# Kernel tuning notes

Measured on AMD Instinct MI355X. Metric: run time of the kernel, lower is better.

Reference implementation:

```python
import jax, jax.numpy as jnp
import numpy as np

L0, L1, L2 = 32, 16, 8
NS, NB = 512, 256
CUT = 7.0
N, E, G = 16384, 131072, 16
FEAT = L0 + 3 * L1 + 5 * L2  # 120


def setup_inputs() -> dict:
    key = jax.random.key(0)
    ks = jax.random.split(key, 16)
    rn = lambda k, s, sc=1.0: jax.random.normal(k, s, jnp.float32) * sc
    inp = {}
    inp['nodes'] = rn(ks[0], (N, FEAT))
    inp['pos'] = rn(ks[1], (N, 3)) * 5.0
    inp['cell'] = rn(ks[2], (G, 3, 3))
    inp['edge_shift'] = rn(ks[3], (E, 3))
    # tensor-product path weights (e3nn FullyConnectedTensorProduct, uvw mode)
    inp['W0'] = rn(ks[4], (L0, L0, NS))
    inp['W1'] = rn(ks[5], (L1, L1, NS))
    inp['W2'] = rn(ks[6], (L2, L2, NS))
    inp['ln_g'] = jnp.ones((NS,), jnp.float32)
    inp['ln_b'] = jnp.zeros((NS,), jnp.float32)
    inp['df_w1'] = rn(ks[7], (NB, 1024), NB ** -0.5)
    inp['df_b1'] = jnp.zeros((1024,), jnp.float32)
    inp['df_w2'] = rn(ks[8], (1024, NS), 1024 ** -0.5)
    inp['df_b2'] = jnp.zeros((NS,), jnp.float32)
    inp['mi_w1'] = rn(ks[9], (NS, 1024), NS ** -0.5)
    inp['mi_b1'] = jnp.zeros((1024,), jnp.float32)
    inp['mi_w2'] = rn(ks[10], (1024, 1024), 1024 ** -0.5)
    inp['mi_b2'] = jnp.zeros((1024,), jnp.float32)
    inp['mo_w'] = rn(ks[11], (1024, 1), 1024 ** -0.5)
    inp['mo_b'] = jnp.zeros((1,), jnp.float32)
    inp['edge_index'] = jax.random.randint(ks[12], (2, E), 0, N)
    inp['batch_vec'] = jnp.sort(jax.random.randint(ks[13], (N,), 0, G))
    return inp


def _split_irreps(x):
    x0 = x[:, :L0]                                   # (E, L0) scalars 0e
    x1 = x[:, L0:L0 + 3 * L1].reshape(-1, L1, 3)      # (E, L1, 3) vectors 1o
    x2 = x[:, L0 + 3 * L1:].reshape(-1, L2, 5)        # (E, L2, 5) 2e
    return x0, x1, x2


def reference(nodes, pos, cell, edge_shift, W0, W1, W2, ln_g, ln_b,
              df_w1, df_b1, df_w2, df_b2, mi_w1, mi_b1, mi_w2, mi_b2,
              mo_w, mo_b, edge_index, batch_vec):
    src, dst = edge_index[0], edge_index[1]
    # periodic-image translation vector per edge
    bcell = cell[batch_vec[src]]                      # (E,3,3)
    tvec = jnp.einsum('ei,eij->ej', edge_shift, bcell)
    radvec = pos[dst] - pos[src] + tvec               # (E,3)
    dist = jnp.linalg.norm(radvec, axis=1, keepdims=True)  # (E,1)
    r = 1.0 / (dist + 1e-6)
    # Bessel radial embedding with cutoff CUT, NB basis functions
    n = jnp.arange(1, NB + 1, dtype=jnp.float32)
    emb = jnp.sqrt(2.0 / CUT) * jnp.sin(n * jnp.pi * r / CUT) / r  # (E,NB)
    distfilter = jax.nn.silu(emb @ df_w1 + df_b1) @ df_w2 + df_b2  # (E,NS)

    # symmetrized fully-connected tensor product -> 0e scalars
    # 0.5*(tp(xs,xd)+tp(xd,xs)) == contraction of euv with symmetrized W
    xs0, xs1, xs2 = _split_irreps(nodes[src])
    xd0, xd1, xd2 = _split_irreps(nodes[dst])
    fan = jnp.sqrt(jnp.float32(L0 * L0 + L1 * L1 + L2 * L2))  # element path norm
    sym = lambda W: 0.5 * (W + W.transpose(1, 0, 2))
    e0 = jnp.einsum('eu,ev->euv', xs0, xd0)
    mixed = jnp.einsum('euv,uvw->ew', e0, sym(W0)) / fan
    e1 = jnp.einsum('eui,evi->euv', xs1, xd1)
    mixed = mixed + jnp.einsum('euv,uvw->ew', e1, sym(W1)) / (fan * jnp.sqrt(3.0))
    e2 = jnp.einsum('eui,evi->euv', xs2, xd2)
    mixed = mixed + jnp.einsum('euv,uvw->ew', e2, sym(W2)) / (fan * jnp.sqrt(5.0))

    # LayerNorm over numscalars
    mu = jnp.mean(mixed, axis=-1, keepdims=True)
    var = jnp.mean((mixed - mu) ** 2, axis=-1, keepdims=True)
    mixednorm = (mixed - mu) * jax.lax.rsqrt(var + 1e-5) * ln_g + ln_b

    reg = mixednorm * distfilter
    h = jax.nn.silu(reg @ mi_w1 + mi_b1)
    h = jax.nn.silu(h @ mi_w2 + mi_b2)
    return h @ mo_w + mo_b  # (E,1)
```

## Files before the change

kernel.cpp:

```cpp
#include <hip/hip_runtime.h>

#define EE 131072
#define NNODE 16384
#define FEAT 120
#define NS 512
#define NB 256
#define KCAT 1344

typedef unsigned short u16;
typedef __bf16 bf16x8 __attribute__((ext_vector_type(8)));
typedef float f32x4 __attribute__((ext_vector_type(4)));
typedef unsigned short ushort8 __attribute__((ext_vector_type(8)));

__device__ __forceinline__ float b2f(u16 u) {
  union { unsigned int i; float f; } x; x.i = ((unsigned int)u) << 16; return x.f;
}
__device__ __forceinline__ u16 f2b(float f) {
  union { float f; unsigned int i; } x; x.f = f;
  unsigned int lsb = (x.i >> 16) & 1u;
  x.i += 0x7fffu + lsb;
  return (u16)(x.i >> 16);
}
__device__ __forceinline__ u16 f2b_fast(float f) {
  __bf16 h = (__bf16)f;
  union { __bf16 h; u16 u; } x; x.h = h; return x.u;
}
__device__ __forceinline__ float rdany(const void* p, long i, int f32) {
  return f32 ? ((const float*)p)[i] : b2f(((const u16*)p)[i]);
}

__device__ __forceinline__ void gload16(const u16* g, u16* l) {
  __builtin_amdgcn_global_load_lds(
      (__attribute__((address_space(1))) void*)(u16*)g,
      (__attribute__((address_space(3))) void*)l, 16, 0, 0);
}

__global__ void detect_k(const u16* __restrict__ nodes, int* __restrict__ flag) {
  __shared__ int cnt;
  if (threadIdx.x == 0) cnt = 0;
  __syncthreads();
  u16 v = nodes[threadIdx.x];
  int e = (v >> 7) & 0xFF;
  if (e >= 0x48) atomicAdd(&cnt, 1);
  __syncthreads();
  if (threadIdx.x == 0) *flag = (cnt >= 16) ? 1 : 0;
}

__global__ __launch_bounds__(256) void convert_k(const void* __restrict__ src,
                                                 u16* __restrict__ dst, long n,
                                                 const int* __restrict__ flag) {
  long i = (long)blockIdx.x * 256 + threadIdx.x;
  if (i >= n) return;
  if (*flag)
    dst[i] = f2b(((const float*)src)[i]);
  else
    dst[i] = ((const u16*)src)[i];
}

__global__ __launch_bounds__(256) void transpose_k(const u16* __restrict__ in,
                                                   u16* __restrict__ out, int R, int C) {
  __shared__ u16 tile[32][33];
  int c0 = blockIdx.x * 32, r0 = blockIdx.y * 32;
  int tx = threadIdx.x & 31, ty = threadIdx.x >> 5;
  for (int i = 0; i < 32; i += 8) {
    int r = r0 + ty + i, c = c0 + tx;
    if (r < R && c < C) tile[ty + i][tx] = in[(long)r * C + c];
  }
  __syncthreads();
  for (int i = 0; i < 32; i += 8) {
    int r = r0 + tx, c = c0 + ty + i;
    if (r < R && c < C) out[(long)c * R + r] = tile[tx][ty + i];
  }
}

__global__ __launch_bounds__(256) void build_wcat(const u16* __restrict__ W0,
                                                  const u16* __restrict__ W1,
                                                  const u16* __restrict__ W2,
                                                  u16* __restrict__ wcT) {
  int idx = blockIdx.x * 256 + threadIdx.x;
  if (idx >= NS * KCAT) return;
  int w = idx / KCAT, k = idx - w * KCAT;
  const float fan = 36.66060556f;
  float val;
  if (k < 1024) {
    int u = k >> 5, v = k & 31;
    val = 0.5f * (b2f(W0[(u * 32 + v) * NS + w]) + b2f(W0[(v * 32 + u) * NS + w])) / fan;
  } else if (k < 1280) {
    int j = k - 1024;
    int u = j >> 4, v = j & 15;
    val = 0.5f * (b2f(W1[(u * 16 + v) * NS + w]) + b2f(W1[(v * 16 + u) * NS + w])) /
          (fan * 1.7320508076f);
  } else {
    int j = k - 1280;
    int u = j >> 3, v = j & 7;
    val = 0.5f * (b2f(W2[(u * 8 + v) * NS + w]) + b2f(W2[(v * 8 + u) * NS + w])) /
          (fan * 2.2360679775f);
  }
  wcT[idx] = f2b(val);
}

__global__ __launch_bounds__(256) void edge_prep(
    const u16* __restrict__ nodes, const void* __restrict__ pos, const void* __restrict__ cell,
    const void* __restrict__ shift, const int* __restrict__ eidx, const int* __restrict__ batch,
    u16* __restrict__ emb, u16* __restrict__ ocat, int e0, const int* __restrict__ flag) {
  const int wave = threadIdx.x >> 6, lane = threadIdx.x & 63;
  const int el = blockIdx.x * 4 + wave;
  const int e = e0 + el;
  const int f32 = *flag;
  __shared__ u16 sxs[4][FEAT], sxd[4][FEAT];
  const int src = eidx[e], dst = eidx[EE + e];
  for (int i = lane; i < FEAT; i += 64) {
    sxs[wave][i] = nodes[(long)src * FEAT + i];
    sxd[wave][i] = nodes[(long)dst * FEAT + i];
  }
  __syncthreads();
  const int b = batch[src];
  float s0 = rdany(shift, (long)e * 3, f32), s1 = rdany(shift, (long)e * 3 + 1, f32),
        s2 = rdany(shift, (long)e * 3 + 2, f32);
  float d2 = 0.f;
#pragma unroll
  for (int j = 0; j < 3; j++) {
    float tv = s0 * rdany(cell, b * 9 + j, f32) + s1 * rdany(cell, b * 9 + 3 + j, f32) +
               s2 * rdany(cell, b * 9 + 6 + j, f32);
    float rv = rdany(pos, dst * 3 + j, f32) - rdany(pos, src * 3 + j, f32) + tv;
    d2 += rv * rv;
  }
  float dist = sqrtf(d2);
  float r = 1.0f / (dist + 1e-6f);
  const float c0 = 0.5345224838f;
  const float pi7 = 0.44879895051f;
#pragma unroll
  for (int j = 0; j < 4; j++) {
    int n = lane + 64 * j;
    float val = c0 * sinf((float)(n + 1) * pi7 * r) / r;
    emb[(long)el * NB + n] = f2b(val);
  }
  const u16* xs = sxs[wave];
  const u16* xd = sxd[wave];
  u16* orow = ocat + (long)el * KCAT;
#pragma unroll
  for (int j = 0; j < 16; j++) {
    int k = lane + 64 * j;
    int u = k >> 5, v = k & 31;
    orow[k] = f2b(b2f(xs[u]) * b2f(xd[v]));
  }
#pragma unroll
  for (int j = 0; j < 4; j++) {
    int k = lane + 64 * j;
    int u = k >> 4, v = k & 15;
    float s = 0.f;
#pragma unroll
    for (int i = 0; i < 3; i++) s += b2f(xs[32 + u * 3 + i]) * b2f(xd[32 + v * 3 + i]);
    orow[1024 + k] = f2b(s);
  }
  {
    int u = lane >> 3, v = lane & 7;
    float s = 0.f;
#pragma unroll
    for (int i = 0; i < 5; i++) s += b2f(xs[80 + u * 5 + i]) * b2f(xd[80 + v * 5 + i]);
    orow[1280 + lane] = f2b(s);
  }
}

#define STGA(buf, h, part, kk)                                             \
  gload16(Ag + ((h)*128 + (part)*64) * (long)K + (kk),                      \
          &lA[buf][(h)*8192 + (part)*4096 + tid * 8])
#define STGB(buf, h, part, kk)                                             \
  gload16(Bg + ((h)*128 + (part)*64) * (long)K + (kk),                      \
          &lB[buf][(h)*8192 + (part)*4096 + tid * 8])
#define RDA(buf, fm, ks)                                                   \
  (*(const bf16x8*)&lA[buf][((((wm * 128 + (fm)*16 + row_l) << 7) +        \
                              (ks)*64 + kq16) >> 1)])
#define RDB(buf, fn, ks)                                                   \
  (*(const bf16x8*)&lB[buf][((((wn * 64 + (fn)*16 + row_l) << 7) +         \
                              (ks)*64 + kq16) >> 1)])
#define MF16(a, b, c) __builtin_amdgcn_mfma_f32_16x16x32_bf16(a, b, c, 0, 0, 0)
#define MFQ(mh, nh)                                                        \
  do {                                                                     \
    _Pragma("unroll") for (int f = 0; f < 4; f++)                          \
        _Pragma("unroll") for (int g = 0; g < 2; g++)                      \
            _Pragma("unroll") for (int ks = 0; ks < 2; ks++)               \
                acc[(mh)*4 + f][(nh)*2 + g] =                              \
        MF16(af[f][ks], bf[(nh)*2 + g][ks], acc[(mh)*4 + f][(nh)*2 + g]);  \
  } while (0)

template <int ACT, int OF32, int HEAD>
__global__ __launch_bounds__(512, 2) void gemm_bt(const u16* __restrict__ A,
                                                  const u16* __restrict__ BT,
                                                  const u16* __restrict__ bias,
                                                  void* __restrict__ Cv,
                                                  const u16* __restrict__ hw,
                                                  float* __restrict__ outf, int N, int K) {
  __shared__ __align__(16) u16 lA[2][16384];
  __shared__ __align__(16) u16 lB[2][16384];
  const int tid = threadIdx.x;
  const int lane = tid & 63;
  const int wave = tid >> 6;
  const int wm = wave >> 2, wn = wave & 3;
  const int row_l = lane & 15;
  const int kq16 = ((lane >> 4) * 16) ^ ((lane & 4) << 3);

  const int nbn = N >> 8;
  int idx = blockIdx.x;
  if ((gridDim.x & 7) == 0) {
    int per = gridDim.x >> 3;
    idx = (blockIdx.x & 7) * per + (blockIdx.x >> 3);
  }
  const int mi = idx / nbn;
  const int ni = idx - mi * nbn;
  const long m0 = (long)mi * 256;
  const int n0 = ni << 8;
  const int nk = K >> 6;

  const int srow = tid >> 3;
  const int gseg = (tid & 7) ^ (((tid >> 5) & 1) << 1);
  const u16* Ag = A + (m0 + srow) * (long)K + gseg * 8;
  const u16* Bg = BT + (long)(n0 + srow) * K + gseg * 8;

  f32x4 acc[8][4];
#pragma unroll
  for (int i = 0; i < 8; i++)
#pragma unroll
    for (int j = 0; j < 4; j++)
#pragma unroll
      for (int q = 0; q < 4; q++) acc[i][j][q] = 0.f;

  STGA(0, 0, 0, 0); STGA(0, 0, 1, 0); STGA(0, 1, 0, 0); STGA(0, 1, 1, 0);
  STGB(0, 0, 0, 0); STGB(0, 0, 1, 0); STGB(0, 1, 0, 0); STGB(0, 1, 1, 0);
  if (nk > 1) {
    STGB(1, 0, 0, 64); STGB(1, 0, 1, 64); STGB(1, 1, 0, 64); STGB(1, 1, 1, 64);
    STGA(1, 0, 0, 64); STGA(1, 0, 1, 64);
    asm volatile("s_waitcnt vmcnt(6)" ::: "memory");
  } else {
    asm volatile("s_waitcnt vmcnt(0)" ::: "memory");
  }
  __builtin_amdgcn_s_barrier();

  bf16x8 af[4][2], bf[4][2];

  for (int t = 0; t < nk; ++t) {
    const int cur = t & 1, nxt = cur ^ 1;
    const int kN = (t + 1) << 6;
    const int kN2 = (t + 2) << 6;
    const bool pA = (t + 1) < nk;
    const bool p2 = (t + 2) < nk;

#pragma unroll
    for (int f = 0; f < 4; f++) { af[f][0] = RDA(cur, f, 0); af[f][1] = RDA(cur, f, 1); }
#pragma unroll
    for (int g = 0; g < 2; g++) { bf[g][0] = RDB(cur, g, 0); bf[g][1] = RDB(cur, g, 1); }
    if (pA) { STGA(nxt, 1, 0, kN); STGA(nxt, 1, 1, kN); }
    __builtin_amdgcn_s_barrier();
    asm volatile("s_waitcnt lgkmcnt(0)" ::: "memory");
    __builtin_amdgcn_s_setprio(1);
    MFQ(0, 0);
    __builtin_amdgcn_s_setprio(0);
    __builtin_amdgcn_s_barrier();

#pragma unroll
    for (int g = 0; g < 2; g++) { bf[2 + g][0] = RDB(cur, 2 + g, 0); bf[2 + g][1] = RDB(cur, 2 + g, 1); }
    __builtin_amdgcn_s_barrier();
    asm volatile("s_waitcnt lgkmcnt(0)" ::: "memory");
    __builtin_amdgcn_s_setprio(1);
    MFQ(0, 1);
    __builtin_amdgcn_s_setprio(0);
    __builtin_amdgcn_s_barrier();

#pragma unroll
    for (int f = 0; f < 4; f++) { af[f][0] = RDA(cur, 4 + f, 0); af[f][1] = RDA(cur, 4 + f, 1); }
    if (p2) { STGB(cur, 0, 0, kN2); STGB(cur, 0, 1, kN2); }
    __builtin_amdgcn_s_barrier();
    asm volatile("s_waitcnt lgkmcnt(0)" ::: "memory");
    __builtin_amdgcn_s_setprio(1);
    MFQ(1, 0);
    __builtin_amdgcn_s_setprio(0);
    __builtin_amdgcn_s_barrier();

    if (p2) {
      STGB(cur, 1, 0, kN2); STGB(cur, 1, 1, kN2);
      STGA(cur, 0, 0, kN2); STGA(cur, 0, 1, kN2);
    }
    __builtin_amdgcn_s_setprio(1);
    MFQ(1, 1);
    __builtin_amdgcn_s_setprio(0);
    if (p2)
      asm volatile("s_waitcnt vmcnt(6)" ::: "memory");
    else
      asm volatile("s_waitcnt vmcnt(0)" ::: "memory");
    __builtin_amdgcn_s_barrier();
  }

  const int rql = (lane >> 4) * 2;
  const int cl = lane & 15;
  float* Cf = (float*)Cv;
  u16* Cb = (u16*)Cv;
  if (HEAD) {
    float bv[4], hv[4];
#pragma unroll
    for (int g = 0; g < 4; g++) {
      const int col = n0 + wn * 64 + g * 16 + cl;
      bv[g] = b2f(bias[col]);
      hv[g] = b2f(hw[col]);
    }
#pragma unroll
    for (int fm = 0; fm < 8; fm++) {
#pragma unroll
      for (int q = 0; q < 4; q++) {
        float s = 0.f;
#pragma unroll
        for (int g = 0; g < 4; g++) {
          float v = acc[fm][g][q] + bv[g];
          if (ACT) v = __fdividef(v, 1.0f + __expf(-v));
          s += v * hv[g];
        }
        s += __shfl_xor(s, 1);
        s += __shfl_xor(s, 2);
        s += __shfl_xor(s, 4);
        s += __shfl_xor(s, 8);
        if (cl == 0) {
          long row = m0 + wm * 128 + fm * 16 + rql * 2 + q;
          atomicAdd(&outf[row], s);
        }
      }
    }
  } else {
#pragma unroll
    for (int fm = 0; fm < 8; fm++) {
#pragma unroll
      for (int g = 0; g < 4; g++) {
        const int col = n0 + wn * 64 + g * 16 + cl;
        const float bvv = bias ? b2f(bias[col]) : 0.0f;
#pragma unroll
        for (int q = 0; q < 4; q++) {
          long row = m0 + wm * 128 + fm * 16 + rql * 2 + q;
          float v = acc[fm][g][q] + bvv;
          if (ACT) v = __fdividef(v, 1.0f + __expf(-v));
          if (OF32)
            Cf[row * N + col] = v;
          else
            Cb[row * N + col] = f2b_fast(v);
        }
      }
    }
  }
}

__global__ __launch_bounds__(256) void ln_mul_k(const float* __restrict__ mixed,
                                                const u16* __restrict__ g,
                                                const u16* __restrict__ bvec,
                                                u16* __restrict__ dfreg) {
  const int wave = threadIdx.x >> 6, lane = threadIdx.x & 63;
  const long e = (long)blockIdx.x * 4 + wave;
  const float* row = mixed + e * NS;
  float x[8];
  f32x4 v0 = *(const f32x4*)&row[lane * 8];
  f32x4 v1 = *(const f32x4*)&row[lane * 8 + 4];
#pragma unroll
  for (int j = 0; j < 4; j++) { x[j] = v0[j]; x[4 + j] = v1[j]; }
  float s = 0.f, sq = 0.f;
#pragma unroll
  for (int j = 0; j < 8; j++) { s += x[j]; sq += x[j] * x[j]; }
  for (int o = 32; o; o >>= 1) { s += __shfl_xor(s, o); sq += __shfl_xor(sq, o); }
  float mu = s * (1.0f / 512.0f);
  float var = sq * (1.0f / 512.0f) - mu * mu;
  float rstd = rsqrtf(var + 1e-5f);
  u16* drow = dfreg + e * NS;
  ushort8 dv = *(const ushort8*)&drow[lane * 8];
  ushort8 ov;
#pragma unroll
  for (int j = 0; j < 8; j++) {
    int c = lane * 8 + j;
    float val = (x[j] - mu) * rstd * b2f(g[c]) + b2f(bvec[c]);
    ov[j] = f2b(val * b2f(dv[j]));
  }
  *(ushort8*)&drow[lane * 8] = ov;
}

__global__ __launch_bounds__(256) void head_finish(const float* __restrict__ outf,
                                                   const u16* __restrict__ b,
                                                   void* __restrict__ out,
                                                   const int* __restrict__ flag) {
  int e = blockIdx.x * 256 + threadIdx.x;
  float v = outf[e] + b2f(b[0]);
  if (*flag)
    ((float*)out)[e] = v;
  else
    ((u16*)out)[e] = f2b(v);
}

extern "C" void kernel_launch(void* const* d_in, const int* in_sizes, int n_in, void* d_out,
                              int out_size, void* d_ws, size_t ws_size, hipStream_t stream) {
  const int* eidx = (const int*)d_in[19];
  const int* batch = (const int*)d_in[20];

  char* ws = (char*)d_ws;
  size_t off = 0;
  auto alloc = [&](size_t bytes) {
    char* p = ws + off;
    off += (bytes + 255) & ~(size_t)255;
    return p;
  };

  int* flag = (int*)alloc(256);
  float* outf = (float*)alloc((size_t)EE * 4);

  detect_k<<<1, 256, 0, stream>>>((const u16*)d_in[0], flag);

  u16* cv[19];
  for (int i = 0; i < 19; i++) {
    long n = in_sizes[i];
    cv[i] = (u16*)alloc((size_t)n * 2);
    convert_k<<<(int)((n + 255) / 256), 256, 0, stream>>>(d_in[i], cv[i], n, flag);
  }
  const u16* nodes = cv[0];
  const u16* W0 = cv[4];
  const u16* W1 = cv[5];
  const u16* W2 = cv[6];
  const u16* ln_g = cv[7];
  const u16* ln_b = cv[8];
  const u16* df_w1 = cv[9];
  const u16* df_b1 = cv[10];
  const u16* df_w2 = cv[11];
  const u16* df_b2 = cv[12];
  const u16* mi_w1 = cv[13];
  const u16* mi_b1 = cv[14];
  const u16* mi_w2 = cv[15];
  const u16* mi_b2 = cv[16];
  const u16* mo_w = cv[17];
  const u16* mo_b = cv[18];

  u16* w1T = (u16*)alloc(1024 * 256 * 2);
  u16* w2T = (u16*)alloc(512 * 1024 * 2);
  u16* m1T = (u16*)alloc(1024 * 512 * 2);
  u16* m2T = (u16*)alloc((size_t)1024 * 1024 * 2);
  u16* wcT = (u16*)alloc((size_t)NS * KCAT * 2);

  int nchunk = 1;
  while (nchunk < 64) {
    size_t CHs = (size_t)(EE / nchunk);
    size_t need = off + CHs * 6272 + 8192;
    if (need <= ws_size) break;
    nchunk <<= 1;
  }
  const int CH = EE / nchunk;

  u16* ocat = (u16*)alloc((size_t)CH * KCAT * 2);
  u16* emb = (u16*)alloc((size_t)CH * NB * 2);
  u16* h1 = (u16*)alloc((size_t)CH * 1024 * 2);
  u16* dfb = (u16*)alloc((size_t)CH * NS * 2);
  u16* h2 = ocat;
  float* mixed = (float*)h1;

  transpose_k<<<dim3(1024 / 32, 256 / 32), 256, 0, stream>>>(df_w1, w1T, 256, 1024);
  transpose_k<<<dim3(512 / 32, 1024 / 32), 256, 0, stream>>>(df_w2, w2T, 1024, 512);
  transpose_k<<<dim3(1024 / 32, 512 / 32), 256, 0, stream>>>(mi_w1, m1T, 512, 1024);
  transpose_k<<<dim3(1024 / 32, 1024 / 32), 256, 0, stream>>>(mi_w2, m2T, 1024, 1024);
  build_wcat<<<(NS * KCAT + 255) / 256, 256, 0, stream>>>(W0, W1, W2, wcT);

  hipMemsetAsync(outf, 0, (size_t)EE * 4, stream);

  const int RB = CH / 256;
  for (int c = 0; c < nchunk; c++) {
    const int eb = c * CH;
    edge_prep<<<CH / 4, 256, 0, stream>>>(nodes, d_in[1], d_in[2], d_in[3], eidx, batch, emb,
                                          ocat, eb, flag);

    gemm_bt<1, 0, 0><<<RB * 4, 512, 0, stream>>>(emb, w1T, df_b1, h1, nullptr, nullptr, 1024, 256);
    gemm_bt<0, 0, 0><<<RB * 2, 512, 0, stream>>>(h1, w2T, df_b2, dfb, nullptr, nullptr, 512, 1024);

    gemm_bt<0, 1, 0><<<RB * 2, 512, 0, stream>>>(ocat, wcT, nullptr, mixed, nullptr, nullptr, 512,
                                                 1344);

    ln_mul_k<<<CH / 4, 256, 0, stream>>>(mixed, ln_g, ln_b, dfb);

    gemm_bt<1, 0, 0><<<RB * 4, 512, 0, stream>>>(dfb, m1T, mi_b1, h2, nullptr, nullptr, 1024, 512);
    gemm_bt<1, 0, 1><<<RB * 4, 512, 0, stream>>>(h2, m2T, mi_b2, nullptr, mo_w, outf + eb, 1024,
                                                 1024);
  }
  head_finish<<<EE / 256, 256, 0, stream>>>(outf, mo_b, d_out, flag);
}
```

Baseline: 1.509 ms.

## Simplify GEMM main loop to full-tile prefetch with XOR-swizzled LDS layout

Replaces the four-phase interleaved GEMM loop, with its many barriers and partial-tile staging, by a simpler double-buffered schedule. Each iteration issues all 64 MFMAs, then one __syncthreads, then stages tile t+2 into the current buffer and preloads every A/B fragment for the next tile into registers. The LDS layout moves to a full 8-way row XOR swizzle on both the global-to-LDS write and the fragment read, to cut bank conflicts. The cost is more fragment registers held live and coarser overlap, since the __syncthreads likely drains outstanding global loads each iteration.

```diff
diff --git a/kernel.cpp b/kernel.cpp
--- a/kernel.cpp
+++ b/kernel.cpp
@@ -162,26 +162,37 @@
   }
 }
 
-#define STGA(buf, h, part, kk)                                             \
-  gload16(Ag + ((h)*128 + (part)*64) * (long)K + (kk),                      \
-          &lA[buf][(h)*8192 + (part)*4096 + tid * 8])
-#define STGB(buf, h, part, kk)                                             \
-  gload16(Bg + ((h)*128 + (part)*64) * (long)K + (kk),                      \
-          &lB[buf][(h)*8192 + (part)*4096 + tid * 8])
-#define RDA(buf, fm, ks)                                                   \
-  (*(const bf16x8*)&lA[buf][((((wm * 128 + (fm)*16 + row_l) << 7) +        \
-                              (ks)*64 + kq16) >> 1)])
-#define RDB(buf, fn, ks)                                                   \
-  (*(const bf16x8*)&lB[buf][((((wn * 64 + (fn)*16 + row_l) << 7) +         \
-                              (ks)*64 + kq16) >> 1)])
+#define STAGE(buf, kk)                                                         \
+  do {                                                                         \
+    _Pragma("unroll") for (int p = 0; p < 4; p++)                              \
+        gload16(Ag + ((p)*64) * (long)K + (kk), &lA[(buf)][(p)*4096 + tid*8]); \
+    _Pragma("unroll") for (int p = 0; p < 4; p++)                              \
+        gload16(Bg + ((p)*64) * (long)K + (kk), &lB[(buf)][(p)*4096 + tid*8]); \
+  } while (0)
+#define RDA(buf, fm, ks)                                                       \
+  (*(const bf16x8*)((const char*)&lA[(buf)][0] +                               \
+                    ((wm * 128 + (fm)*16 + row_l) * 128 + ((ks) ? ir1 : ir0))))
+#define RDB(buf, fn, ks)                                                       \
+  (*(const bf16x8*)((const char*)&lB[(buf)][0] +                               \
+                    ((wn * 64 + (fn)*16 + row_l) * 128 + ((ks) ? ir1 : ir0))))
+#define LOADFRAGS(buf)                                                         \
+  do {                                                                         \
+    _Pragma("unroll") for (int f = 0; f < 4; f++) {                            \
+      af[f][0] = RDA(buf, f, 0); af[f][1] = RDA(buf, f, 1); }                  \
+    _Pragma("unroll") for (int g = 0; g < 4; g++) {                            \
+      bfr[g][0] = RDB(buf, g, 0); bfr[g][1] = RDB(buf, g, 1); }                \
+    _Pragma("unroll") for (int f = 4; f < 8; f++) {                            \
+      af[f][0] = RDA(buf, f, 0); af[f][1] = RDA(buf, f, 1); }                  \
+  } while (0)
 #define MF16(a, b, c) __builtin_amdgcn_mfma_f32_16x16x32_bf16(a, b, c, 0, 0, 0)
-#define MFQ(mh, nh)                                                        \
-  do {                                                                     \
-    _Pragma("unroll") for (int f = 0; f < 4; f++)                          \
-        _Pragma("unroll") for (int g = 0; g < 2; g++)                      \
-            _Pragma("unroll") for (int ks = 0; ks < 2; ks++)               \
-                acc[(mh)*4 + f][(nh)*2 + g] =                              \
-        MF16(af[f][ks], bf[(nh)*2 + g][ks], acc[(mh)*4 + f][(nh)*2 + g]);  \
+#define MFQ(mh, nh)                                                            \
+  do {                                                                         \
+    _Pragma("unroll") for (int f = 0; f < 4; f++)                              \
+        _Pragma("unroll") for (int g = 0; g < 2; g++)                          \
+            _Pragma("unroll") for (int ks = 0; ks < 2; ks++)                   \
+                acc[(mh)*4 + f][(nh)*2 + g] =                                  \
+        MF16(af[(mh)*4 + f][ks], bfr[(nh)*2 + g][ks],                          \
+             acc[(mh)*4 + f][(nh)*2 + g]);                                     \
   } while (0)
 
 template <int ACT, int OF32, int HEAD>
@@ -198,7 +209,10 @@
   const int wave = tid >> 6;
   const int wm = wave >> 2, wn = wave & 3;
   const int row_l = lane & 15;
-  const int kq16 = ((lane >> 4) * 16) ^ ((lane & 4) << 3);
+  const int kq16 = (lane >> 4) << 4;
+  const int swz = (row_l & 7) << 4;
+  const int ir0 = kq16 ^ swz;
+  const int ir1 = (64 + kq16) ^ swz;
 
   const int nbn = N >> 8;
   int idx = blockIdx.x;
@@ -213,7 +227,7 @@
   const int nk = K >> 6;
 
   const int srow = tid >> 3;
-  const int gseg = (tid & 7) ^ (((tid >> 5) & 1) << 1);
+  const int gseg = (tid & 7) ^ (srow & 7);
   const u16* Ag = A + (m0 + srow) * (long)K + gseg * 8;
   const u16* Bg = BT + (long)(n0 + srow) * K + gseg * 8;
 
@@ -225,69 +239,30 @@
 #pragma unroll
       for (int q = 0; q < 4; q++) acc[i][j][q] = 0.f;
 
-  STGA(0, 0, 0, 0); STGA(0, 0, 1, 0); STGA(0, 1, 0, 0); STGA(0, 1, 1, 0);
-  STGB(0, 0, 0, 0); STGB(0, 0, 1, 0); STGB(0, 1, 0, 0); STGB(0, 1, 1, 0);
+  bf16x8 af[8][2], bfr[4][2];
+
+  STAGE(0, 0);
   if (nk > 1) {
-    STGB(1, 0, 0, 64); STGB(1, 0, 1, 64); STGB(1, 1, 0, 64); STGB(1, 1, 1, 64);
-    STGA(1, 0, 0, 64); STGA(1, 0, 1, 64);
-    asm volatile("s_waitcnt vmcnt(6)" ::: "memory");
+    STAGE(1, 64);
+    asm volatile("s_waitcnt vmcnt(8)" ::: "memory");
   } else {
     asm volatile("s_waitcnt vmcnt(0)" ::: "memory");
   }
   __builtin_amdgcn_s_barrier();
-
-  bf16x8 af[4][2], bf[4][2];
+  asm volatile("" ::: "memory");
+  LOADFRAGS(0);
 
   for (int t = 0; t < nk; ++t) {
     const int cur = t & 1, nxt = cur ^ 1;
-    const int kN = (t + 1) << 6;
-    const int kN2 = (t + 2) << 6;
-    const bool pA = (t + 1) < nk;
-    const bool p2 = (t + 2) < nk;
-
-#pragma unroll
-    for (int f = 0; f < 4; f++) { af[f][0] = RDA(cur, f, 0); af[f][1] = RDA(cur, f, 1); }
-#pragma unroll
-    for (int g = 0; g < 2; g++) { bf[g][0] = RDB(cur, g, 0); bf[g][1] = RDB(cur, g, 1); }
-    if (pA) { STGA(nxt, 1, 0, kN); STGA(nxt, 1, 1, kN); }
-    __builtin_amdgcn_s_barrier();
-    asm volatile("s_waitcnt lgkmcnt(0)" ::: "memory");
     __builtin_amdgcn_s_setprio(1);
     MFQ(0, 0);
-    __builtin_amdgcn_s_setprio(0);
-    __builtin_amdgcn_s_barrier();
-
-#pragma unroll
-    for (int g = 0; g < 2; g++) { bf[2 + g][0] = RDB(cur, 2 + g, 0); bf[2 + g][1] = RDB(cur, 2 + g, 1); }
-    __builtin_amdgcn_s_barrier();
-    asm volatile("s_waitcnt lgkmcnt(0)" ::: "memory");
-    __builtin_amdgcn_s_setprio(1);
     MFQ(0, 1);
-    __builtin_amdgcn_s_setprio(0);
-    __builtin_amdgcn_s_barrier();
-
-#pragma unroll
-    for (int f = 0; f < 4; f++) { af[f][0] = RDA(cur, 4 + f, 0); af[f][1] = RDA(cur, 4 + f, 1); }
-    if (p2) { STGB(cur, 0, 0, kN2); STGB(cur, 0, 1, kN2); }
-    __builtin_amdgcn_s_barrier();
-    asm volatile("s_waitcnt lgkmcnt(0)" ::: "memory");
-    __builtin_amdgcn_s_setprio(1);
     MFQ(1, 0);
-    __builtin_amdgcn_s_setprio(0);
-    __builtin_amdgcn_s_barrier();
-
-    if (p2) {
-      STGB(cur, 1, 0, kN2); STGB(cur, 1, 1, kN2);
-      STGA(cur, 0, 0, kN2); STGA(cur, 0, 1, kN2);
-    }
-    __builtin_amdgcn_s_setprio(1);
     MFQ(1, 1);
     __builtin_amdgcn_s_setprio(0);
-    if (p2)
-      asm volatile("s_waitcnt vmcnt(6)" ::: "memory");
-    else
-      asm volatile("s_waitcnt vmcnt(0)" ::: "memory");
-    __builtin_amdgcn_s_barrier();
+    __syncthreads();
+    if (t + 2 < nk) STAGE(cur, (t + 2) * 64);
+    if (t + 1 < nk) LOADFRAGS(nxt);
   }
 
   const int rql = (lane >> 4) * 2;
```

Measured after the change: 1.462 ms. 1.03x faster.
